# Kernel optimization log

Measured on AMD Instinct MI355X. Metric: run time of the kernel, lower is better.

The kernel has to match this reference:

```python
import jax, jax.numpy as jnp
import numpy as np

DECAY = 0.99
EPS = 1e-05
TEMP = 1.0


def setup_inputs() -> dict:
    key = jax.random.key(0)
    k1, k2, k3 = jax.random.split(key, 3)
    B, T, D, C = 64, 512, 256, 1024
    x = jax.random.normal(k1, (B, T, D), dtype=jnp.float32)
    embed = jax.random.normal(k2, (1, C, D), dtype=jnp.float32)
    embed_avg = jax.random.normal(k3, (1, C, D), dtype=jnp.float32)
    cluster_size = jnp.ones((1, C), dtype=jnp.float32)
    return {"x": x, "embed": embed, "embed_avg": embed_avg, "cluster_size": cluster_size}


def reference(x, embed, embed_avg, cluster_size):
    B, T, D = x.shape
    H, C, _ = embed.shape  # H = num_codebooks = 1
    flatten = x.reshape(H, B * T, D)  # pack_one 'h * d'
    e = jax.lax.stop_gradient(embed)  # learnable_codebook = False

    dist = (2.0 * jnp.einsum('hnd,hcd->hnc', flatten, e)
            - jnp.sum(flatten * flatten, axis=-1, keepdims=True)
            - jnp.sum(e * e, axis=-1)[:, None, :])  # [h, N, C]

    # gumbel_sample: deterministic argmax + straight-through one-hot
    embed_ind = jnp.argmax(dist, axis=-1)  # [h, N]
    probs = jax.nn.softmax(dist / TEMP, axis=-1)
    hard = jax.nn.one_hot(embed_ind, C, dtype=dist.dtype)
    embed_onehot = probs + jax.lax.stop_gradient(hard - probs)  # [h, N, C]

    # quantize via onehot matmul (training path)
    quantize = jnp.einsum('hnc,hcd->hnd', embed_onehot, e).reshape(B, T, D)

    # EMA codebook update
    cs_new = DECAY * cluster_size + (1.0 - DECAY) * embed_onehot.sum(axis=1)  # [h, C]
    embed_sum = jnp.einsum('hnd,hnc->hcd', flatten, embed_onehot)  # [h, C, D]
    ea_new = DECAY * embed_avg + (1.0 - DECAY) * embed_sum
    n = jnp.sum(cs_new, axis=-1, keepdims=True)
    cs_smoothed = (cs_new + EPS) / (n + C * EPS) * n  # laplace smoothing * n
    embed_norm = ea_new / cs_smoothed[..., None]  # new codebook [h, C, D]

    return (quantize, embed_ind.reshape(B, T), embed_norm, cs_new)
```

## Files before the change

kernel.cpp:

```cpp
#include <hip/hip_runtime.h>
#include <cstdint>

#define DECAY 0.99f
#define OMD   0.01f
#define EPSV  1e-5f

constexpr int N_PTS   = 32768;
constexpr int D_DIM   = 256;
constexpr int C_CODES = 1024;
constexpr int NKT     = 12;
constexpr int AP      = 512;
constexpr int BP      = 512;

constexpr int PG = 4;
constexpr int PK = 8;
constexpr int LCAP = 8192;

typedef _Float16 half8  __attribute__((ext_vector_type(8)));
typedef _Float16 half4v __attribute__((ext_vector_type(4)));
typedef float    floatx4 __attribute__((ext_vector_type(4)));

constexpr size_t WS_ENORM = 0;
constexpr size_t WS_FCNT  = 1024;
constexpr size_t WS_PCNT  = 2048;
constexpr size_t WS_XNORM = 8192;
constexpr size_t WS_CAND4 = 40960;
constexpr size_t WS_FLAGR = WS_CAND4 + 1048576;
constexpr size_t WS_CAND2 = WS_FLAGR + 32768;
constexpr size_t WS_A16   = WS_CAND2 + 1048576;
constexpr size_t WS_B16   = WS_A16 + 8388608;
constexpr size_t WS_TOTAL_FLOATS = WS_B16 + 262144;

__device__ __forceinline__ void async_copy16(const void* g, void* s) {
    __builtin_amdgcn_global_load_lds(
        (const __attribute__((address_space(1))) unsigned int*)(uintptr_t)g,
        (__attribute__((address_space(3))) unsigned int*)(uintptr_t)s, 16, 0, 0);
}

__global__ __launch_bounds__(256) void vq_prep(const float* __restrict__ X,
                                               const float* __restrict__ E,
                                               _Float16* __restrict__ A,
                                               _Float16* __restrict__ B,
                                               float* __restrict__ enorm,
                                               float* __restrict__ xnorm,
                                               int* __restrict__ fcnt) {
    if (blockIdx.x < 8192) {
        int i = blockIdx.x * 256 + threadIdx.x;
        int n = i >> 6, kq = (i & 63) * 4;
        float4 v = reinterpret_cast<const float4*>(X)[i];
        _Float16 h0 = (_Float16)v.x, h1 = (_Float16)v.y, h2 = (_Float16)v.z, h3 = (_Float16)v.w;
        _Float16 l0 = (_Float16)(v.x - (float)h0), l1 = (_Float16)(v.y - (float)h1);
        _Float16 l2 = (_Float16)(v.z - (float)h2), l3 = (_Float16)(v.w - (float)h3);
        half4v hi = {h0, h1, h2, h3};
        half4v lo = {l0, l1, l2, l3};
        _Float16* row = A + (size_t)n * AP;
        *reinterpret_cast<half4v*>(row + kq)       = hi;
        *reinterpret_cast<half4v*>(row + 256 + kq) = lo;
        float s = v.x * v.x + v.y * v.y + v.z * v.z + v.w * v.w;
        int lane = threadIdx.x & 63;
#pragma unroll
        for (int off = 32; off > 0; off >>= 1) s += __shfl_down(s, off, 64);
        if (lane == 0) xnorm[n] = s;
    } else {
        if (blockIdx.x == 8192 && threadIdx.x == 0) *fcnt = 0;
        int i = (blockIdx.x - 8192) * 256 + threadIdx.x;
        int c = i >> 6, kq = (i & 63) * 4;
        float4 v = reinterpret_cast<const float4*>(E)[i];
        _Float16 h0 = (_Float16)v.x, h1 = (_Float16)v.y, h2 = (_Float16)v.z, h3 = (_Float16)v.w;
        _Float16 l0 = (_Float16)(v.x - (float)h0), l1 = (_Float16)(v.y - (float)h1);
        _Float16 l2 = (_Float16)(v.z - (float)h2), l3 = (_Float16)(v.w - (float)h3);
        half4v hi = {h0, h1, h2, h3};
        half4v lo = {l0, l1, l2, l3};
        _Float16* row = B + (size_t)c * BP;
        *reinterpret_cast<half4v*>(row + kq)       = hi;
        *reinterpret_cast<half4v*>(row + 256 + kq) = lo;
        float s = v.x * v.x + v.y * v.y + v.z * v.z + v.w * v.w;
        int lane = threadIdx.x & 63;
#pragma unroll
        for (int off = 32; off > 0; off >>= 1) s += __shfl_down(s, off, 64);
        if (lane == 0) enorm[c] = s;
    }
}

__global__ __launch_bounds__(256) void vq_enorm(const float* __restrict__ E,
                                                float* __restrict__ enorm) {
    int c    = blockIdx.x * 4 + (threadIdx.x >> 6);
    int lane = threadIdx.x & 63;
    float4 v = reinterpret_cast<const float4*>(E)[c * 64 + lane];
    float s  = v.x * v.x + v.y * v.y + v.z * v.z + v.w * v.w;
#pragma unroll
    for (int off = 32; off > 0; off >>= 1) s += __shfl_down(s, off, 64);
    if (lane == 0) enorm[c] = s;
}

__global__ __launch_bounds__(256, 2) void vq_gemm1(
    const _Float16* __restrict__ A, const _Float16* __restrict__ B,
    const float* __restrict__ enorm, float4* __restrict__ cand4) {
    __shared__ _Float16 As[128 * 64];
    __shared__ _Float16 Bs[256 * 64];

    const int L  = blockIdx.x;
    const int ct = (L >> 3) & 3;
    const int rt = (L & 7) | ((L >> 5) << 3);
    const int n0  = rt * 128;
    const int cb0 = ct * 256;

    const int tid = threadIdx.x;
    const int w   = tid >> 6;
    const int l   = tid & 63;

    const int srow = l >> 3;
    const int sq   = (l & 7) ^ srow;

    floatx4 acc[4][8] = {};

    for (int kt = 0; kt < 4; ++kt) {
        const int k0 = kt * 64;
        __syncthreads();
#pragma unroll
        for (int t = 0; t < 4; ++t) {
            int rr = w * 32 + t * 8;
            const _Float16* ga = A + (size_t)(n0 + rr + srow) * AP + k0 + sq * 8;
            async_copy16(ga, &As[rr * 64]);
        }
#pragma unroll
        for (int t = 0; t < 8; ++t) {
            int rr = w * 64 + t * 8;
            const _Float16* gb = B + (size_t)(cb0 + rr + srow) * BP + k0 + sq * 8;
            async_copy16(gb, &Bs[rr * 64]);
        }
        __syncthreads();
#pragma unroll
        for (int kk = 0; kk < 2; ++kk) {
            half8 af[4], bf[8];
            int qa = kk * 4 + (l >> 4);
#pragma unroll
            for (int i = 0; i < 4; ++i) {
                int row = (w & 1) * 64 + 16 * i + (l & 15);
                af[i] = *reinterpret_cast<const half8*>(&As[row * 64 + (qa ^ (row & 7)) * 8]);
            }
#pragma unroll
            for (int j = 0; j < 8; ++j) {
                int crow = (w >> 1) * 128 + 16 * j + (l & 15);
                bf[j] = *reinterpret_cast<const half8*>(&Bs[crow * 64 + (qa ^ (crow & 7)) * 8]);
            }
#pragma unroll
            for (int i = 0; i < 4; ++i)
#pragma unroll
                for (int j = 0; j < 8; ++j)
                    acc[i][j] = __builtin_amdgcn_mfma_f32_16x16x32_f16(af[i], bf[j], acc[i][j], 0, 0, 0);
        }
    }

    const int colbase = cb0 + (w >> 1) * 128 + (l & 15);
    float en[8];
#pragma unroll
    for (int j = 0; j < 8; ++j) en[j] = enorm[colbase + 16 * j];

#pragma unroll
    for (int i = 0; i < 4; ++i) {
#pragma unroll
        for (int reg = 0; reg < 4; ++reg) {
            float bv = -3.4e38f, sv = -3.4e38f;
            int   bi = 0x7fffffff;
#pragma unroll
            for (int j = 0; j < 8; ++j) {
                float v = 2.0f * acc[i][j][reg] - en[j];
                int   c = colbase + 16 * j;
                if (v > bv || (v == bv && c < bi)) { sv = bv; bv = v; bi = c; }
                else sv = fmaxf(sv, v);
            }
#pragma unroll
            for (int s = 1; s < 16; s <<= 1) {
                float ov  = __shfl_xor(bv, s, 64);
                int   oi  = __shfl_xor(bi, s, 64);
                float osv = __shfl_xor(sv, s, 64);
                if (ov > bv || (ov == bv && oi < bi)) { sv = fmaxf(bv, osv); bv = ov; bi = oi; }
                else sv = fmaxf(sv, ov);
            }
            if ((l & 15) == 0) {
                int row = n0 + (w & 1) * 64 + 16 * i + (l >> 4) * 4 + reg;
                cand4[(size_t)row * 8 + ct * 2 + (w >> 1)] =
                    make_float4(bv, (float)bi, sv, 0.0f);
            }
        }
    }
}

__global__ __launch_bounds__(256) void vq_merge3f(
    const float4* __restrict__ cand4, const float* __restrict__ E,
    const float* __restrict__ enorm, const float* __restrict__ xnorm,
    float* __restrict__ quant, float* __restrict__ indout,
    int* __restrict__ flagrows, int* __restrict__ fcnt) {
    __shared__ int   rowsel[64];
    __shared__ float emred[256];
    const int tid = threadIdx.x;
    const int n0  = blockIdx.x * 64;

    float em = fmaxf(fmaxf(enorm[tid], enorm[tid + 256]),
                     fmaxf(enorm[tid + 512], enorm[tid + 768]));
    emred[tid] = em;
    __syncthreads();
    for (int st = 128; st > 0; st >>= 1) {
        if (tid < st) emred[tid] = fmaxf(emred[tid], emred[tid + st]);
        __syncthreads();
    }
    const float emax = emred[0];

    if (tid < 64) {
        int r = n0 + tid;
        float b1 = -3.4e38f, b2 = -3.4e38f;
        int   i1 = 0x7fffffff;
#pragma unroll
        for (int t = 0; t < 8; ++t) {
            float4 cv = cand4[(size_t)r * 8 + t];
            int ci = (int)cv.y;
            if (cv.x > b1 || (cv.x == b1 && ci < i1)) { b2 = fmaxf(b1, cv.z); b1 = cv.x; i1 = ci; }
            else b2 = fmaxf(b2, cv.x);
        }
        i1 &= (C_CODES - 1);
        rowsel[tid] = i1;
        indout[r]   = (float)i1;
        float T = 0.00390625f * sqrtf(xnorm[r] * emax) + 0.5f;
        if (b1 - b2 <= T) { int p = atomicAdd(fcnt, 1); flagrows[p] = r; }
    }
    __syncthreads();

    const float4* E4 = reinterpret_cast<const float4*>(E);
    float4*       Q4 = reinterpret_cast<float4*>(quant);
    const int lane = tid & 63;
#pragma unroll
    for (int it = 0; it < 16; ++it) {
        int r   = (tid >> 6) + 4 * it;
        int idx = rowsel[r];
        Q4[(n0 + r) * 64 + lane] = E4[idx * 64 + lane];
    }
}

__global__ __launch_bounds__(256, 2) void vq_gemm2(
    const _Float16* __restrict__ A, const _Float16* __restrict__ B,
    const float* __restrict__ enorm, const int* __restrict__ flagrows,
    const int* __restrict__ fcnt, float2* __restrict__ cand2) {
    const int fc = *fcnt;

    const int L      = blockIdx.x;
    const int within = L >> 3;
    const int ct     = within & 7;
    const int rt     = (L & 7) | ((within >> 3) << 3);
    const int n0     = rt * 128;
    if (n0 >= fc) return;
    const int cb0    = ct * 128;

    __shared__ _Float16 As[128 * 64];
    __shared__ _Float16 Bs[128 * 64];

    const int tid = threadIdx.x;
    const int w   = tid >> 6;
    const int l   = tid & 63;
    const int srow = l >> 3;
    const int sq   = (l & 7) ^ srow;

    int grow[4];
#pragma unroll
    for (int t = 0; t < 4; ++t) {
        int slot = n0 + w * 32 + t * 8 + srow;
        int r    = (slot < fc) ? flagrows[slot] : 0;
        grow[t]  = r & (N_PTS - 1);
    }

    floatx4 acc[4][4] = {};

    for (int kt = 0; kt < NKT; ++kt) {
        const int ka = ((kt < 8) ? (kt & 3) : (kt - 4)) * 64;
        const int kb = (kt < 4) ? kt * 64 : (kt < 8 ? 256 + (kt - 4) * 64 : (kt - 8) * 64);
        __syncthreads();
#pragma unroll
        for (int t = 0; t < 4; ++t) {
            int rr = w * 32 + t * 8;
            const _Float16* ga = A + (size_t)grow[t] * AP + ka + sq * 8;
            async_copy16(ga, &As[rr * 64]);
            const _Float16* gb = B + (size_t)(cb0 + rr + srow) * BP + kb + sq * 8;
            async_copy16(gb, &Bs[rr * 64]);
        }
        __syncthreads();
#pragma unroll
        for (int kk = 0; kk < 2; ++kk) {
            half8 af[4], bf[4];
            int qa = kk * 4 + (l >> 4);
#pragma unroll
            for (int i = 0; i < 4; ++i) {
                int row  = (w & 1) * 64 + 16 * i + (l & 15);
                af[i] = *reinterpret_cast<const half8*>(&As[row * 64 + (qa ^ (row & 7)) * 8]);
                int crow = (w >> 1) * 64 + 16 * i + (l & 15);
                bf[i] = *reinterpret_cast<const half8*>(&Bs[crow * 64 + (qa ^ (crow & 7)) * 8]);
            }
#pragma unroll
            for (int i = 0; i < 4; ++i)
#pragma unroll
                for (int j = 0; j < 4; ++j)
                    acc[i][j] = __builtin_amdgcn_mfma_f32_16x16x32_f16(af[i], bf[j], acc[i][j], 0, 0, 0);
        }
    }

    const int colbase = cb0 + (w >> 1) * 64 + (l & 15);
    float en[4];
#pragma unroll
    for (int j = 0; j < 4; ++j) en[j] = enorm[colbase + 16 * j];

#pragma unroll
    for (int i = 0; i < 4; ++i) {
#pragma unroll
        for (int reg = 0; reg < 4; ++reg) {
            float bv = -3.4e38f;
            int   bi = 0x7fffffff;
#pragma unroll
            for (int j = 0; j < 4; ++j) {
                float v = 2.0f * acc[i][j][reg] - en[j];
                int   c = colbase + 16 * j;
                if (v > bv || (v == bv && c < bi)) { bv = v; bi = c; }
            }
#pragma unroll
            for (int s = 1; s < 16; s <<= 1) {
                float ov = __shfl_xor(bv, s, 64);
                int   oi = __shfl_xor(bi, s, 64);
                if (ov > bv || (ov == bv && oi < bi)) { bv = ov; bi = oi; }
            }
            if ((l & 15) == 0) {
                int slot = n0 + (w & 1) * 64 + 16 * i + (l >> 4) * 4 + reg;
                cand2[(size_t)slot * 16 + ct * 2 + (w >> 1)] = make_float2(bv, (float)bi);
            }
        }
    }
}

__global__ __launch_bounds__(256) void vq_patch(
    const float2* __restrict__ cand2, const int* __restrict__ flagrows,
    const int* __restrict__ fcnt, const float* __restrict__ E,
    float* __restrict__ quant, float* __restrict__ indout) {
    int fc = *fcnt;
    if (fc > N_PTS) fc = N_PTS;
    const int s0 = blockIdx.x * 64;
    if (s0 >= fc) return;

    __shared__ int rowsel[64];
    __shared__ int rowid[64];
    const int tid = threadIdx.x;
    if (tid < 64) {
        int s = s0 + tid;
        if (s < fc) {
            int r = flagrows[s] & (N_PTS - 1);
            float bv = -3.4e38f;
            int   bi = 0x7fffffff;
#pragma unroll
            for (int t = 0; t < 16; ++t) {
                float2 cv = cand2[(size_t)s * 16 + t];
                int ci = (int)cv.y;
                if (cv.x > bv || (cv.x == bv && ci < bi)) { bv = cv.x; bi = ci; }
            }
            bi &= (C_CODES - 1);
            rowsel[tid] = bi;
            rowid[tid]  = r;
            indout[r]   = (float)bi;
        } else {
            rowsel[tid] = -1;
            rowid[tid]  = 0;
        }
    }
    __syncthreads();

    const float4* E4 = reinterpret_cast<const float4*>(E);
    float4*       Q4 = reinterpret_cast<float4*>(quant);
    const int lane = tid & 63;
#pragma unroll
    for (int it = 0; it < 16; ++it) {
        int rs  = (tid >> 6) + 4 * it;
        int idx = rowsel[rs];
        if (idx >= 0) Q4[(size_t)rowid[rs] * 64 + lane] = E4[idx * 64 + lane];
    }
}

__global__ __launch_bounds__(256) void vq_part(
    const float* __restrict__ X, const float* __restrict__ indf,
    float* __restrict__ P, int* __restrict__ pcnt) {
    __shared__ int list[LCAP];
    __shared__ int cnt[PK];
    __shared__ int lcnt;
    const int cg = blockIdx.x;
    const int g  = blockIdx.y;
    const int t  = threadIdx.x;
    if (t == 0) lcnt = 0;
    if (t < PK) cnt[t] = 0;
    __syncthreads();

    const float4* I4 = reinterpret_cast<const float4*>(indf);
    float4 v[8];
#pragma unroll
    for (int j = 0; j < 8; ++j)
        v[j] = I4[g * 2048 + j * 256 + t];

#pragma unroll
    for (int j = 0; j < 8; ++j) {
        int base = (g * 2048 + j * 256 + t) * 4;
        int k0 = (int)v[j].x, k1 = (int)v[j].y, k2 = (int)v[j].z, k3 = (int)v[j].w;
        if ((k0 >> 3) == cg) { int p = atomicAdd(&lcnt, 1); atomicAdd(&cnt[k0 & 7], 1); if (p < LCAP) list[p] = ((base + 0) << 3) | (k0 & 7); }
        if ((k1 >> 3) == cg) { int p = atomicAdd(&lcnt, 1); atomicAdd(&cnt[k1 & 7], 1); if (p < LCAP) list[p] = ((base + 1) << 3) | (k1 & 7); }
        if ((k2 >> 3) == cg) { int p = atomicAdd(&lcnt, 1); atomicAdd(&cnt[k2 & 7], 1); if (p < LCAP) list[p] = ((base + 2) << 3) | (k2 & 7); }
        if ((k3 >> 3) == cg) { int p = atomicAdd(&lcnt, 1); atomicAdd(&cnt[k3 & 7], 1); if (p < LCAP) list[p] = ((base + 3) << 3) | (k3 & 7); }
    }
    __syncthreads();

    int m = lcnt; if (m > LCAP) m = LCAP;
    float acc[PK] = {0, 0, 0, 0, 0, 0, 0, 0};
    int r = 0;
    for (; r + 8 <= m; r += 8) {
        int e[8];
        float val[8];
#pragma unroll
        for (int q = 0; q < 8; ++q) e[q] = list[r + q];
#pragma unroll
        for (int q = 0; q < 8; ++q) val[q] = X[(size_t)(e[q] >> 3) * D_DIM + t];
#pragma unroll
        for (int q = 0; q < 8; ++q) {
            int k = e[q] & 7;
#pragma unroll
            for (int kk = 0; kk < PK; ++kk) acc[kk] += (k == kk) ? val[q] : 0.0f;
        }
    }
    for (; r < m; ++r) {
        int e = list[r];
        float val = X[(size_t)(e >> 3) * D_DIM + t];
        int k = e & 7;
#pragma unroll
        for (int kk = 0; kk < PK; ++kk) acc[kk] += (k == kk) ? val : 0.0f;
    }

#pragma unroll
    for (int kk = 0; kk < PK; ++kk)
        P[((size_t)g * C_CODES + cg * PK + kk) * D_DIM + t] = acc[kk];
    if (t < PK) pcnt[g * C_CODES + cg * PK + t] = cnt[t];
}

__global__ __launch_bounds__(256) void vq_comb(
    const float* __restrict__ P, const int* __restrict__ pcnt,
    const float* __restrict__ ea, const float* __restrict__ cs_in,
    float* __restrict__ emb_norm, float* __restrict__ cs_out) {
    __shared__ float red[256];
    const int c = blockIdx.x;
    const int t = threadIdx.x;
    red[t] = cs_in[t] + cs_in[t + 256] + cs_in[t + 512] + cs_in[t + 768];
    __syncthreads();
    for (int st = 128; st > 0; st >>= 1) {
        if (t < st) red[t] += red[t + st];
        __syncthreads();
    }
    const float cssum = red[0];

    float s = 0.0f;
#pragma unroll
    for (int g = 0; g < PG; ++g)
        s += P[((size_t)g * C_CODES + c) * D_DIM + t];
    int total = pcnt[c] + pcnt[C_CODES + c] + pcnt[2 * C_CODES + c] + pcnt[3 * C_CODES + c];
    float cs    = DECAY * cs_in[c] + OMD * (float)total;
    float ntot  = DECAY * cssum + OMD * (float)N_PTS;
    float denom = (cs + EPSV) / (ntot + (float)C_CODES * EPSV) * ntot;
    emb_norm[(size_t)c * D_DIM + t] =
        (DECAY * ea[(size_t)c * D_DIM + t] + OMD * s) / denom;
    if (t == 0) cs_out[c] = cs;
}

__global__ __launch_bounds__(256) void vq_main_fb(
    const float* __restrict__ X, const float* __restrict__ E,
    const float* __restrict__ enorm,
    float* __restrict__ quant, float* __restrict__ indout,
    float* __restrict__ counts, float* __restrict__ esum) {
    constexpr int BN = 64, BC = 64, BK = 32, PADR = 68;
    __shared__ float As[BK * PADR];
    __shared__ float Bs[BK * PADR];
    __shared__ float redv[BN * 16];
    __shared__ int   redi[BN * 16];
    __shared__ int   rowsel[BN];

    const int tid = threadIdx.x;
    const int n0  = blockIdx.x * BN;
    const int tr  = tid >> 4;
    const int tc  = tid & 15;
    const int sr  = tid >> 2;
    const int sk  = tid & 3;

    const float4* X4 = reinterpret_cast<const float4*>(X);
    const float4* E4 = reinterpret_cast<const float4*>(E);

    float best[4];
    int   bidx[4];
#pragma unroll
    for (int i = 0; i < 4; i++) { best[i] = -3.4e38f; bidx[i] = 0; }

    for (int c0 = 0; c0 < C_CODES; c0 += BC) {
        float acc[4][4] = {};
        for (int k0 = 0; k0 < D_DIM; k0 += BK) {
            __syncthreads();
#pragma unroll
            for (int it = 0; it < 2; ++it) {
                int   k4 = sk + 4 * it;
                float4 av = X4[(n0 + sr) * 64 + (k0 >> 2) + k4];
                float4 bv = E4[(c0 + sr) * 64 + (k0 >> 2) + k4];
                int kk = k4 * 4;
                As[(kk + 0) * PADR + sr] = av.x;
                As[(kk + 1) * PADR + sr] = av.y;
                As[(kk + 2) * PADR + sr] = av.z;
                As[(kk + 3) * PADR + sr] = av.w;
                Bs[(kk + 0) * PADR + sr] = bv.x;
                Bs[(kk + 1) * PADR + sr] = bv.y;
                Bs[(kk + 2) * PADR + sr] = bv.z;
                Bs[(kk + 3) * PADR + sr] = bv.w;
            }
            __syncthreads();
#pragma unroll
            for (int k = 0; k < BK; ++k) {
                float4 a = *reinterpret_cast<const float4*>(&As[k * PADR + 4 * tr]);
                float4 b = *reinterpret_cast<const float4*>(&Bs[k * PADR + 4 * tc]);
                acc[0][0] += a.x * b.x; acc[0][1] += a.x * b.y;
                acc[0][2] += a.x * b.z; acc[0][3] += a.x * b.w;
                acc[1][0] += a.y * b.x; acc[1][1] += a.y * b.y;
                acc[1][2] += a.y * b.z; acc[1][3] += a.y * b.w;
                acc[2][0] += a.z * b.x; acc[2][1] += a.z * b.y;
                acc[2][2] += a.z * b.z; acc[2][3] += a.z * b.w;
                acc[3][0] += a.w * b.x; acc[3][1] += a.w * b.y;
                acc[3][2] += a.w * b.z; acc[3][3] += a.w * b.w;
            }
        }
        float4 en = *reinterpret_cast<const float4*>(&enorm[c0 + 4 * tc]);
        float enj[4] = {en.x, en.y, en.z, en.w};
#pragma unroll
        for (int i = 0; i < 4; i++)
#pragma unroll
            for (int j = 0; j < 4; j++) {
                float v = 2.0f * acc[i][j] - enj[j];
                int   c = c0 + 4 * tc + j;
                if (v > best[i]) { best[i] = v; bidx[i] = c; }
            }
    }

    __syncthreads();
#pragma unroll
    for (int i = 0; i < 4; i++) {
        redv[(4 * tr + i) * 16 + tc] = best[i];
        redi[(4 * tr + i) * 16 + tc] = bidx[i];
    }
    __syncthreads();
    if (tid < BN) {
        float bv = redv[tid * 16];
        int   bi = redi[tid * 16];
        for (int t = 1; t < 16; t++) {
            float v  = redv[tid * 16 + t];
            int   id = redi[tid * 16 + t];
            if (v > bv || (v == bv && id < bi)) { bv = v; bi = id; }
        }
        rowsel[tid] = bi;
        indout[n0 + tid] = (float)bi;
        unsafeAtomicAdd(&counts[bi], 1.0f);
    }
    __syncthreads();

    float4*   Q4   = reinterpret_cast<float4*>(quant);
    const int lane = tid & 63;
#pragma unroll
    for (int it = 0; it < 16; ++it) {
        int r   = (tid >> 6) + 4 * it;
        int idx = rowsel[r];
        float4 ev = E4[idx * 64 + lane];
        Q4[(n0 + r) * 64 + lane] = ev;
        float4 xv = X4[(n0 + r) * 64 + lane];
        float* dst = &esum[idx * D_DIM + lane * 4];
        unsafeAtomicAdd(dst + 0, xv.x);
        unsafeAtomicAdd(dst + 1, xv.y);
        unsafeAtomicAdd(dst + 2, xv.z);
        unsafeAtomicAdd(dst + 3, xv.w);
    }
}

__global__ __launch_bounds__(1024) void vq_fin1(const float* __restrict__ cs_in,
                                                const float* __restrict__ counts,
                                                float* __restrict__ cs_out,
                                                float* __restrict__ denom) {
    __shared__ float red[1024];
    int   c  = threadIdx.x;
    float cs = DECAY * cs_in[c] + OMD * counts[c];
    cs_out[c] = cs;
    red[c]    = cs;
    __syncthreads();
    for (int s = 512; s > 0; s >>= 1) {
        if (c < s) red[c] += red[c + s];
        __syncthreads();
    }
    float ntot = red[0];
    denom[c] = (cs + EPSV) / (ntot + (float)C_CODES * EPSV) * ntot;
}

__global__ __launch_bounds__(256) void vq_fin2(const float* __restrict__ ea,
                                               const float* __restrict__ esum,
                                               const float* __restrict__ denom,
                                               float* __restrict__ out) {
    int i = blockIdx.x * 256 + threadIdx.x;
    int c = i >> 6;
    float4 a = reinterpret_cast<const float4*>(ea)[i];
    float4 s = reinterpret_cast<const float4*>(esum)[i];
    float  d = denom[c];
    float4 o;
    o.x = (DECAY * a.x + OMD * s.x) / d;
    o.y = (DECAY * a.y + OMD * s.y) / d;
    o.z = (DECAY * a.z + OMD * s.z) / d;
    o.w = (DECAY * a.w + OMD * s.w) / d;
    reinterpret_cast<float4*>(out)[i] = o;
}

extern "C" void kernel_launch(void* const* d_in, const int* in_sizes, int n_in,
                              void* d_out, int out_size, void* d_ws, size_t ws_size,
                              hipStream_t stream) {
    const float* x            = (const float*)d_in[0];
    const float* embed        = (const float*)d_in[1];
    const float* embed_avg    = (const float*)d_in[2];
    const float* cluster_size = (const float*)d_in[3];

    float* out      = (float*)d_out;
    float* quant    = out;
    float* ind      = out + (size_t)N_PTS * D_DIM;
    float* emb_norm = ind + N_PTS;
    float* cs_out   = emb_norm + (size_t)C_CODES * D_DIM;

    float* ws    = (float*)d_ws;
    float* enorm = ws + WS_ENORM;

    if (ws_size >= WS_TOTAL_FLOATS * sizeof(float)) {
        int*      fcnt  = (int*)(ws + WS_FCNT);
        int*      pcnt  = (int*)(ws + WS_PCNT);
        float*    xnorm = ws + WS_XNORM;
        float4*   cand4 = (float4*)(ws + WS_CAND4);
        float*    P     = ws + WS_CAND4;
        int*      flagr = (int*)(ws + WS_FLAGR);
        float2*   cand2 = (float2*)(ws + WS_CAND2);
        _Float16* A16   = (_Float16*)(ws + WS_A16);
        _Float16* B16   = (_Float16*)(ws + WS_B16);

        vq_prep<<<8448, 256, 0, stream>>>(x, embed, A16, B16, enorm, xnorm, fcnt);
        vq_gemm1<<<1024, 256, 0, stream>>>(A16, B16, enorm, cand4);
        vq_merge3f<<<N_PTS / 64, 256, 0, stream>>>(cand4, embed, enorm, xnorm,
                                                   quant, ind, flagr, fcnt);
        vq_gemm2<<<2048, 256, 0, stream>>>(A16, B16, enorm, flagr, fcnt, cand2);
        vq_patch<<<N_PTS / 64, 256, 0, stream>>>(cand2, flagr, fcnt, embed, quant, ind);
        vq_part<<<dim3(C_CODES / PK, PG), 256, 0, stream>>>(x, ind, P, pcnt);
        vq_comb<<<C_CODES, 256, 0, stream>>>(P, pcnt, embed_avg, cluster_size,
                                             emb_norm, cs_out);
    } else {
        vq_enorm<<<C_CODES / 4, 256, 0, stream>>>(embed, enorm);
        float* countsf = ws + WS_CAND4;
        float* esum    = ws + WS_CAND4 + 1024;
        float* denom   = ws + WS_A16;
        hipMemsetAsync(countsf, 0, (1024 + (size_t)C_CODES * D_DIM) * sizeof(float), stream);
        vq_main_fb<<<N_PTS / 64, 256, 0, stream>>>(x, embed, enorm, quant, ind, countsf, esum);
        vq_fin1<<<1, 1024, 0, stream>>>(cluster_size, countsf, cs_out, denom);
        vq_fin2<<<(C_CODES * D_DIM / 4) / 256, 256, 0, stream>>>(embed_avg, esum, denom, emb_norm);
    }
}
```

Measured before the change: 225.7 us.

## Pack top-2 distance keys into ordered uints with DPP reduction, split partition into more groups

The gemm1 epilogue now encodes each distance as an order-preserving uint and packs the inverted code index into its low 10 bits. A top-2 is then tracked with integer max/min and reduced across 16 lanes with DPP moves instead of three-value shuffles with tie-breaking compares. Dropping the low mantissa bits loses some precision, so the merge threshold for flagging rows to exact recompute is widened to cover it. Separately, the EMA partition kernel uses 8 point groups instead of 4 with a smaller LDS list, which raises parallelism at the cost of more partial sums to reduce.

```diff
diff --git a/kernel.cpp b/kernel.cpp
--- a/kernel.cpp
+++ b/kernel.cpp
@@ -12,9 +12,9 @@
 constexpr int AP      = 512;
 constexpr int BP      = 512;
 
-constexpr int PG = 4;
+constexpr int PG = 8;
 constexpr int PK = 8;
-constexpr int LCAP = 8192;
+constexpr int LCAP = 4096;
 
 typedef _Float16 half8  __attribute__((ext_vector_type(8)));
 typedef _Float16 half4v __attribute__((ext_vector_type(4)));
@@ -22,9 +22,9 @@
 
 constexpr size_t WS_ENORM = 0;
 constexpr size_t WS_FCNT  = 1024;
-constexpr size_t WS_PCNT  = 2048;
-constexpr size_t WS_XNORM = 8192;
-constexpr size_t WS_CAND4 = 40960;
+constexpr size_t WS_XNORM = 2048;
+constexpr size_t WS_PCNT  = 34816;
+constexpr size_t WS_CAND4 = 43008;
 constexpr size_t WS_FLAGR = WS_CAND4 + 1048576;
 constexpr size_t WS_CAND2 = WS_FLAGR + 32768;
 constexpr size_t WS_A16   = WS_CAND2 + 1048576;
@@ -35,6 +35,16 @@
     __builtin_amdgcn_global_load_lds(
         (const __attribute__((address_space(1))) unsigned int*)(uintptr_t)g,
         (__attribute__((address_space(3))) unsigned int*)(uintptr_t)s, 16, 0, 0);
+}
+
+__device__ __forceinline__ unsigned ord_u32(float v) {
+    unsigned s = __float_as_uint(v);
+    unsigned m = (unsigned)((int)s >> 31);
+    return s ^ (m | 0x80000000u);
+}
+__device__ __forceinline__ float ord_dec(unsigned t) {
+    unsigned s = (t & 0x80000000u) ? (t ^ 0x80000000u) : ~t;
+    return __uint_as_float(s);
 }
 
 __global__ __launch_bounds__(256) void vq_prep(const float* __restrict__ X,
@@ -93,6 +103,18 @@
     if (lane == 0) enorm[c] = s;
 }
 
+#define TOP2_DPP(CTRL)                                                          \
+    {                                                                           \
+        unsigned o1 = (unsigned)__builtin_amdgcn_update_dpp((int)k1, (int)k1,   \
+                                                            CTRL, 0xF, 0xF, false); \
+        unsigned o2 = (unsigned)__builtin_amdgcn_update_dpp((int)k2, (int)k2,   \
+                                                            CTRL, 0xF, 0xF, false); \
+        unsigned tmn = o1 < k1 ? o1 : k1;                                       \
+        k1 = o1 > k1 ? o1 : k1;                                                 \
+        k2 = o2 > k2 ? o2 : k2;                                                 \
+        k2 = tmn > k2 ? tmn : k2;                                               \
+    }
+
 __global__ __launch_bounds__(256, 2) void vq_gemm1(
     const _Float16* __restrict__ A, const _Float16* __restrict__ B,
     const float* __restrict__ enorm, float4* __restrict__ cand4) {
@@ -153,35 +175,38 @@
     }
 
     const int colbase = cb0 + (w >> 1) * 128 + (l & 15);
-    float en[8];
-#pragma unroll
-    for (int j = 0; j < 8; ++j) en[j] = enorm[colbase + 16 * j];
+    float    en[8];
+    unsigned idxenc[8];
+#pragma unroll
+    for (int j = 0; j < 8; ++j) {
+        en[j]     = enorm[colbase + 16 * j];
+        idxenc[j] = 1023u - (unsigned)(colbase + 16 * j);
+    }
 
 #pragma unroll
     for (int i = 0; i < 4; ++i) {
 #pragma unroll
         for (int reg = 0; reg < 4; ++reg) {
-            float bv = -3.4e38f, sv = -3.4e38f;
-            int   bi = 0x7fffffff;
+            unsigned k1 = 0u, k2 = 0u;
 #pragma unroll
             for (int j = 0; j < 8; ++j) {
                 float v = 2.0f * acc[i][j][reg] - en[j];
-                int   c = colbase + 16 * j;
-                if (v > bv || (v == bv && c < bi)) { sv = bv; bv = v; bi = c; }
-                else sv = fmaxf(sv, v);
-            }
-#pragma unroll
-            for (int s = 1; s < 16; s <<= 1) {
-                float ov  = __shfl_xor(bv, s, 64);
-                int   oi  = __shfl_xor(bi, s, 64);
-                float osv = __shfl_xor(sv, s, 64);
-                if (ov > bv || (ov == bv && oi < bi)) { sv = fmaxf(bv, osv); bv = ov; bi = oi; }
-                else sv = fmaxf(sv, ov);
-            }
+                unsigned key = (ord_u32(v) & 0xFFFFFC00u) | idxenc[j];
+                unsigned tmn = key < k1 ? key : k1;
+                k1 = key > k1 ? key : k1;
+                k2 = tmn > k2 ? tmn : k2;
+            }
+            TOP2_DPP(0xB1)
+            TOP2_DPP(0x4E)
+            TOP2_DPP(0x141)
+            TOP2_DPP(0x140)
             if ((l & 15) == 0) {
+                unsigned c1 = 1023u - (k1 & 1023u);
+                float v1 = ord_dec(k1 & 0xFFFFFC00u);
+                float v2 = ord_dec(k2 & 0xFFFFFC00u);
                 int row = n0 + (w & 1) * 64 + 16 * i + (l >> 4) * 4 + reg;
                 cand4[(size_t)row * 8 + ct * 2 + (w >> 1)] =
-                    make_float4(bv, (float)bi, sv, 0.0f);
+                    make_float4(v1, (float)c1, v2, 0.0f);
             }
         }
     }
@@ -221,7 +246,8 @@
         i1 &= (C_CODES - 1);
         rowsel[tid] = i1;
         indout[r]   = (float)i1;
-        float T = 0.00390625f * sqrtf(xnorm[r] * emax) + 0.5f;
+        float T = 0.004150390625f * sqrtf(xnorm[r] * emax)
+                + 0.0001220703125f * emax + 0.5f;
         if (b1 - b2 <= T) { int p = atomicAdd(fcnt, 1); flagrows[p] = r; }
     }
     __syncthreads();
@@ -393,14 +419,14 @@
     __syncthreads();
 
     const float4* I4 = reinterpret_cast<const float4*>(indf);
-    float4 v[8];
-#pragma unroll
-    for (int j = 0; j < 8; ++j)
-        v[j] = I4[g * 2048 + j * 256 + t];
-
-#pragma unroll
-    for (int j = 0; j < 8; ++j) {
-        int base = (g * 2048 + j * 256 + t) * 4;
+    float4 v[4];
+#pragma unroll
+    for (int j = 0; j < 4; ++j)
+        v[j] = I4[g * 1024 + j * 256 + t];
+
+#pragma unroll
+    for (int j = 0; j < 4; ++j) {
+        int base = (g * 1024 + j * 256 + t) * 4;
         int k0 = (int)v[j].x, k1 = (int)v[j].y, k2 = (int)v[j].z, k3 = (int)v[j].w;
         if ((k0 >> 3) == cg) { int p = atomicAdd(&lcnt, 1); atomicAdd(&cnt[k0 & 7], 1); if (p < LCAP) list[p] = ((base + 0) << 3) | (k0 & 7); }
         if ((k1 >> 3) == cg) { int p = atomicAdd(&lcnt, 1); atomicAdd(&cnt[k1 & 7], 1); if (p < LCAP) list[p] = ((base + 1) << 3) | (k1 & 7); }
@@ -459,7 +485,9 @@
 #pragma unroll
     for (int g = 0; g < PG; ++g)
         s += P[((size_t)g * C_CODES + c) * D_DIM + t];
-    int total = pcnt[c] + pcnt[C_CODES + c] + pcnt[2 * C_CODES + c] + pcnt[3 * C_CODES + c];
+    int total = 0;
+#pragma unroll
+    for (int g = 0; g < PG; ++g) total += pcnt[g * C_CODES + c];
     float cs    = DECAY * cs_in[c] + OMD * (float)total;
     float ntot  = DECAY * cssum + OMD * (float)N_PTS;
     float denom = (cs + EPSV) / (ntot + (float)C_CODES * EPSV) * ntot;
```

New measurement: 196.8 us. -12.8%, faster.
